# Optimization experiments

Measured on AMD Instinct MI355X. Metric: run time of the kernel, lower is better.

The kernel has to match this reference:

```python
import jax, jax.numpy as jnp
import numpy as np

D_MODEL = 1024
NHEAD = 16
HEAD_DIM = D_MODEL // NHEAD


def setup_inputs() -> dict:
    key = jax.random.key(0)
    ks = jax.random.split(key, 11)
    B, L, D = 4, 2048, D_MODEL
    s = 1.0 / np.sqrt(D)  # ~ torch Linear init scale
    return {
        "queries": jax.random.normal(ks[0], (B, L, D), jnp.float32),
        "keys": jax.random.normal(ks[1], (B, L, D), jnp.float32),
        "values": jax.random.normal(ks[2], (B, L, D), jnp.float32),
        "Wq": jax.random.normal(ks[3], (D, D), jnp.float32) * s,
        "bq": jnp.zeros((D,), jnp.float32),
        "Wk": jax.random.normal(ks[4], (D, D), jnp.float32) * s,
        "bk": jnp.zeros((D,), jnp.float32),
        "Wv": jax.random.normal(ks[5], (D, D), jnp.float32) * s,
        "bv": jnp.zeros((D,), jnp.float32),
        "Wo": jax.random.normal(ks[6], (D, D), jnp.float32) * s,
        "bo": jnp.zeros((D,), jnp.float32),
    }


def reference(queries, keys, values, Wq, bq, Wk, bk, Wv, bv, Wo, bo):
    B, L, D = queries.shape
    H, dh = NHEAD, HEAD_DIM
    # projections (W stored as [in, out])
    q = (queries @ Wq + bq).reshape(B, L, H, dh).transpose(0, 2, 1, 3)  # [B,H,L,dh]
    k = (keys @ Wk + bk).reshape(B, L, H, dh).transpose(0, 2, 1, 3)
    v = (values @ Wv + bv).reshape(B, L, H, dh).transpose(0, 2, 1, 3)
    scores = jnp.einsum("bhqd,bhkd->bhqk", q, k) / jnp.sqrt(jnp.float32(dh))
    attn = jax.nn.softmax(scores, axis=-1)  # dropout p=0 -> identity
    ctx = jnp.einsum("bhqk,bhkd->bhqd", attn, v)
    ctx = ctx.transpose(0, 2, 1, 3).reshape(B, L, D)
    return ctx @ Wo + bo
```

## Files before the change

### kernel.cpp

```cpp
#include <hip/hip_runtime.h>
#include <math.h>


using f32x4 = __attribute__((ext_vector_type(4))) float;
using bf16x8 = __attribute__((ext_vector_type(8))) short;

__device__ __forceinline__ unsigned short f2bf(float x) {
  union { float f; unsigned u; } v; v.f = x;
  unsigned r = v.u + 0x7fff + ((v.u >> 16) & 1);
  return (unsigned short)(r >> 16);
}

__device__ __forceinline__ void g2l16(const void* g, void* l) {
  __builtin_amdgcn_global_load_lds(
      (const __attribute__((address_space(1))) unsigned int*)g,
      (__attribute__((address_space(3))) unsigned int*)l, 16, 0, 0);
}

__global__ __launch_bounds__(256) void wt4_k(const float* __restrict__ W0,
                                             const float* __restrict__ W1,
                                             const float* __restrict__ W2,
                                             const float* __restrict__ W3,
                                             short* __restrict__ WT) {
  __shared__ float t[64][65];
  const int z = blockIdx.z;
  const float* W = z == 0 ? W0 : (z == 1 ? W1 : (z == 2 ? W2 : W3));
  short* hiT = WT + (size_t)z * 1048576;
  const int n0 = blockIdx.x * 64, k0 = blockIdx.y * 64;
  const int tid = threadIdx.x;
  const int r = tid >> 4, c4 = (tid & 15) * 4;
#pragma unroll
  for (int i = 0; i < 4; i++) {
    const int row = r + i * 16;
    const float4 v = *(const float4*)&W[(size_t)(k0 + row) * 1024 + n0 + c4];
    t[c4 + 0][row] = v.x;
    t[c4 + 1][row] = v.y;
    t[c4 + 2][row] = v.z;
    t[c4 + 3][row] = v.w;
  }
  __syncthreads();
#pragma unroll
  for (int i = 0; i < 4; i++) {
    const int row = r + i * 16;
    short4 h;
    h.x = (short)f2bf(t[row][c4 + 0]);
    h.y = (short)f2bf(t[row][c4 + 1]);
    h.z = (short)f2bf(t[row][c4 + 2]);
    h.w = (short)f2bf(t[row][c4 + 3]);
    *(short4*)&hiT[(size_t)(n0 + row) * 1024 + k0 + c4] = h;
  }
}

__global__ __launch_bounds__(256) void cvt3_k(const float* __restrict__ A0,
                                              const float* __restrict__ A1,
                                              const float* __restrict__ A2,
                                              short* __restrict__ X) {
  const int z = blockIdx.y;
  const float* A = z == 0 ? A0 : (z == 1 ? A1 : A2);
  short* Xo = X + (size_t)z * 8388608;
  const int t0 = blockIdx.x * 256 + threadIdx.x;
#pragma unroll 2
  for (int i = t0; i < 1048576; i += 262144) {
    const size_t o = (size_t)i * 8;
    const float4 a = *(const float4*)&A[o];
    const float4 b = *(const float4*)&A[o + 4];
    short tmp[8];
    tmp[0] = (short)f2bf(a.x);
    tmp[1] = (short)f2bf(a.y);
    tmp[2] = (short)f2bf(a.z);
    tmp[3] = (short)f2bf(a.w);
    tmp[4] = (short)f2bf(b.x);
    tmp[5] = (short)f2bf(b.y);
    tmp[6] = (short)f2bf(b.z);
    tmp[7] = (short)f2bf(b.w);
    *(bf16x8*)&Xo[o] = *(const bf16x8*)tmp;
  }
}

__global__ __launch_bounds__(256, 4) void proj3_k(
    const short* __restrict__ X, const short* __restrict__ WT,
    const float* __restrict__ b0, const float* __restrict__ b1,
    const float* __restrict__ b2, short* __restrict__ Obase) {
  __shared__ short smem[64 * 144];
  short* As = smem;
  short* Bs = smem + 4096;

  const int z = blockIdx.z;
  const short* A_g = X + (size_t)z * 8388608;
  const short* B_g = WT + (size_t)z * 1048576;
  const float* bias = z == 0 ? b0 : (z == 1 ? b1 : b2);
  short* outp = Obase + (size_t)z * 8388608;

  const int tid = threadIdx.x;
  const int lane = tid & 63;
  const int wave = tid >> 6;
  const int quad = lane >> 4;
  const int l16 = lane & 15;
  const int m0 = blockIdx.x * 128;
  const int n0 = blockIdx.y * 128;
  const int wm = (wave >> 1) * 64;
  const int wn = (wave & 1) * 64;

  const int srow = tid >> 2;
  const int soff = (tid & 3) * 8;

  f32x4 acc[4][4];
#pragma unroll
  for (int i = 0; i < 4; i++)
#pragma unroll
    for (int j = 0; j < 4; j++) acc[i][j] = f32x4{0.f, 0.f, 0.f, 0.f};

  for (int k0 = 0; k0 < 1024; k0 += 32) {
    __syncthreads();
#pragma unroll
    for (int i = 0; i < 2; i++) {
      const int row = srow + i * 64;
      g2l16(&A_g[(size_t)(m0 + row) * 1024 + k0 + soff], &As[row * 32 + soff]);
      g2l16(&B_g[(size_t)(n0 + row) * 1024 + k0 + soff], &Bs[row * 32 + soff]);
    }
    __syncthreads();

    bf16x8 ah[4], bh[4];
#pragma unroll
    for (int t = 0; t < 4; t++) {
      ah[t] = *(const bf16x8*)&As[(wm + t * 16 + l16) * 32 + quad * 8];
      bh[t] = *(const bf16x8*)&Bs[(wn + t * 16 + l16) * 32 + quad * 8];
    }
#pragma unroll
    for (int tm = 0; tm < 4; tm++)
#pragma unroll
      for (int tn = 0; tn < 4; tn++)
        acc[tm][tn] = __builtin_amdgcn_mfma_f32_16x16x32_bf16(ah[tm], bh[tn], acc[tm][tn], 0, 0, 0);
  }

  float bz[4];
#pragma unroll
  for (int tn = 0; tn < 4; tn++) bz[tn] = bias[n0 + wn + tn * 16 + l16];
  const float sc = (z == 0) ? 0.125f : 1.0f;

  const int b = m0 >> 11;
  const int lbase = m0 & 2047;

  if (z == 2) {
#pragma unroll
    for (int half = 0; half < 2; half++) {
      __syncthreads();
      if ((wave & 1) == half) {
#pragma unroll
        for (int tm = 0; tm < 4; tm++)
#pragma unroll
          for (int tn = 0; tn < 4; tn++)
#pragma unroll
            for (int r = 0; r < 4; r++) {
              const int nl = tn * 16 + l16;
              const int ml = wm + tm * 16 + quad * 4 + r;
              smem[nl * 144 + ml] = (short)f2bf(acc[tm][tn][r] + bz[tn]);
            }
      }
      __syncthreads();
      const int h = (n0 >> 6) + half;
#pragma unroll
      for (int j = 0; j < 4; j++) {
        const int c = tid + j * 256;
        const int d = c >> 4;
        const int mo = (c & 15) * 8;
        *(bf16x8*)&outp[((size_t)((b * 16 + h) * 64 + d)) * 2048 + lbase + mo] =
            *(const bf16x8*)&smem[d * 144 + mo];
      }
    }
  } else {
#pragma unroll
    for (int half = 0; half < 2; half++) {
      __syncthreads();
      if ((wave & 1) == half) {
#pragma unroll
        for (int tm = 0; tm < 4; tm++)
#pragma unroll
          for (int tn = 0; tn < 4; tn++)
#pragma unroll
            for (int r = 0; r < 4; r++) {
              const int ml = wm + tm * 16 + quad * 4 + r;
              const int nl = tn * 16 + l16;
              smem[ml * 72 + nl] = (short)f2bf((acc[tm][tn][r] + bz[tn]) * sc);
            }
      }
      __syncthreads();
      const int h = (n0 >> 6) + half;
#pragma unroll
      for (int j = 0; j < 4; j++) {
        const int c = tid + j * 256;
        const int ml = c >> 3;
        const int off = (c & 7) * 8;
        *(bf16x8*)&outp[((size_t)(b * 16 + h) * 2048 + lbase + ml) * 64 + off] =
            *(const bf16x8*)&smem[ml * 72 + off];
      }
    }
  }
}

__global__ __launch_bounds__(256, 2) void outproj_k(
    const short* __restrict__ A_g, const short* __restrict__ B_g,
    const float* __restrict__ bias, float* __restrict__ out0) {
  __shared__ short As[4096];
  __shared__ short Bs[4096];

  const int tid = threadIdx.x;
  const int lane = tid & 63;
  const int wave = tid >> 6;
  const int quad = lane >> 4;
  const int l16 = lane & 15;
  const int m0 = blockIdx.x * 128;
  const int n0 = blockIdx.y * 128;
  const int wm = (wave >> 1) * 64;
  const int wn = (wave & 1) * 64;
  const int srow = tid >> 2;
  const int soff = (tid & 3) * 8;

  f32x4 acc[4][4];
#pragma unroll
  for (int i = 0; i < 4; i++)
#pragma unroll
    for (int j = 0; j < 4; j++) acc[i][j] = f32x4{0.f, 0.f, 0.f, 0.f};

  for (int k0 = 0; k0 < 1024; k0 += 32) {
    __syncthreads();
#pragma unroll
    for (int i = 0; i < 2; i++) {
      const int row = srow + i * 64;
      g2l16(&A_g[(size_t)(m0 + row) * 1024 + k0 + soff], &As[row * 32 + soff]);
      g2l16(&B_g[(size_t)(n0 + row) * 1024 + k0 + soff], &Bs[row * 32 + soff]);
    }
    __syncthreads();

    bf16x8 ah[4], bh[4];
#pragma unroll
    for (int t = 0; t < 4; t++) {
      ah[t] = *(const bf16x8*)&As[(wm + t * 16 + l16) * 32 + quad * 8];
      bh[t] = *(const bf16x8*)&Bs[(wn + t * 16 + l16) * 32 + quad * 8];
    }
#pragma unroll
    for (int tm = 0; tm < 4; tm++)
#pragma unroll
      for (int tn = 0; tn < 4; tn++)
        acc[tm][tn] = __builtin_amdgcn_mfma_f32_16x16x32_bf16(ah[tm], bh[tn], acc[tm][tn], 0, 0, 0);
  }

  float bz[4];
#pragma unroll
  for (int tn = 0; tn < 4; tn++) bz[tn] = bias[n0 + wn + tn * 16 + l16];

#pragma unroll
  for (int tm = 0; tm < 4; tm++)
#pragma unroll
    for (int tn = 0; tn < 4; tn++) {
      const int n = n0 + wn + tn * 16 + l16;
#pragma unroll
      for (int r = 0; r < 4; r++) {
        const int m = m0 + wm + tm * 16 + quad * 4 + r;
        out0[(size_t)m * 1024 + n] = acc[tm][tn][r] + bz[tn];
      }
    }
}

__global__ __launch_bounds__(256, 4) void attn3_k(const short* __restrict__ Qp,
                                                  const short* __restrict__ Kp,
                                                  const short* __restrict__ Vt,
                                                  short* __restrict__ Ctx) {
  __shared__ short Ks[64 * 72];
  __shared__ short Vs[64 * 72];
  __shared__ short Ps[128 * 72];

  const int tid = threadIdx.x;
  const int lane = tid & 63;
  const int wave = tid >> 6;
  const int quad = lane >> 4;
  const int l16 = lane & 15;
  const int bh = blockIdx.x;
  const int q0 = blockIdx.y * 128;

  const short* Kb = Kp + (size_t)bh * 2048 * 64;
  const short* Vb = Vt + (size_t)bh * 64 * 2048;

  bf16x8 qf[2][2];
#pragma unroll
  for (int s = 0; s < 2; s++) {
    const short* qp =
        Qp + ((size_t)bh * 2048 + q0 + wave * 32 + s * 16 + l16) * 64 + quad * 8;
    qf[s][0] = *(const bf16x8*)qp;
    qf[s][1] = *(const bf16x8*)(qp + 32);
  }

  bf16x8 ones;
#pragma unroll
  for (int j = 0; j < 8; j++) ones[j] = (short)0x3F80;

  f32x4 O[2][4], lacc[2];
#pragma unroll
  for (int s = 0; s < 2; s++) {
    lacc[s] = f32x4{0.f, 0.f, 0.f, 0.f};
#pragma unroll
    for (int jo = 0; jo < 4; jo++) O[s][jo] = f32x4{0.f, 0.f, 0.f, 0.f};
  }

  const int srow0 = tid >> 3, soff = (tid & 7) * 8;
  const int srow1 = (tid + 256) >> 3;

  bf16x8 kreg[2], vreg[2];
  kreg[0] = *(const bf16x8*)&Kb[(size_t)srow0 * 64 + soff];
  kreg[1] = *(const bf16x8*)&Kb[(size_t)srow1 * 64 + soff];
  vreg[0] = *(const bf16x8*)&Vb[(size_t)srow0 * 2048 + soff];
  vreg[1] = *(const bf16x8*)&Vb[(size_t)srow1 * 2048 + soff];

  for (int kt = 0; kt < 32; kt++) {
    __syncthreads();
    *(bf16x8*)&Ks[srow0 * 72 + soff] = kreg[0];
    *(bf16x8*)&Ks[srow1 * 72 + soff] = kreg[1];
    *(bf16x8*)&Vs[srow0 * 72 + soff] = vreg[0];
    *(bf16x8*)&Vs[srow1 * 72 + soff] = vreg[1];
    __syncthreads();

    if (kt < 31) {
      const int nb = (kt + 1) * 64;
      kreg[0] = *(const bf16x8*)&Kb[(size_t)(nb + srow0) * 64 + soff];
      kreg[1] = *(const bf16x8*)&Kb[(size_t)(nb + srow1) * 64 + soff];
      vreg[0] = *(const bf16x8*)&Vb[(size_t)srow0 * 2048 + nb + soff];
      vreg[1] = *(const bf16x8*)&Vb[(size_t)srow1 * 2048 + nb + soff];
    }

#pragma unroll
    for (int s = 0; s < 2; s++) {
      f32x4 sacc[4];
#pragma unroll
      for (int j = 0; j < 4; j++) sacc[j] = f32x4{0.f, 0.f, 0.f, 0.f};
#pragma unroll
      for (int c = 0; c < 2; c++)
#pragma unroll
        for (int j = 0; j < 4; j++) {
          const bf16x8 kf = *(const bf16x8*)&Ks[(j * 16 + l16) * 72 + c * 32 + quad * 8];
          sacc[j] = __builtin_amdgcn_mfma_f32_16x16x32_bf16(qf[s][c], kf, sacc[j], 0, 0, 0);
        }
#pragma unroll
      for (int j = 0; j < 4; j++)
#pragma unroll
        for (int r = 0; r < 4; r++) {
          const float e = __expf(sacc[j][r]);
          Ps[(wave * 32 + s * 16 + quad * 4 + r) * 72 + j * 16 + l16] =
              (short)(__float_as_uint(e) >> 16);
        }
    }

#pragma unroll
    for (int c = 0; c < 2; c++) {
      const bf16x8 pf0 = *(const bf16x8*)&Ps[(wave * 32 + l16) * 72 + c * 32 + quad * 8];
      const bf16x8 pf1 = *(const bf16x8*)&Ps[(wave * 32 + 16 + l16) * 72 + c * 32 + quad * 8];
      lacc[0] = __builtin_amdgcn_mfma_f32_16x16x32_bf16(pf0, ones, lacc[0], 0, 0, 0);
      lacc[1] = __builtin_amdgcn_mfma_f32_16x16x32_bf16(pf1, ones, lacc[1], 0, 0, 0);
#pragma unroll
      for (int jo = 0; jo < 4; jo++) {
        const bf16x8 vf = *(const bf16x8*)&Vs[(jo * 16 + l16) * 72 + c * 32 + quad * 8];
        O[0][jo] = __builtin_amdgcn_mfma_f32_16x16x32_bf16(pf0, vf, O[0][jo], 0, 0, 0);
        O[1][jo] = __builtin_amdgcn_mfma_f32_16x16x32_bf16(pf1, vf, O[1][jo], 0, 0, 0);
      }
    }
  }

  const int b = bh >> 4, h = bh & 15;
#pragma unroll
  for (int s = 0; s < 2; s++)
#pragma unroll
    for (int r = 0; r < 4; r++) {
      const float inv_l = 1.0f / lacc[s][r];
      const size_t row = (size_t)b * 2048 + q0 + wave * 32 + s * 16 + quad * 4 + r;
#pragma unroll
      for (int jo = 0; jo < 4; jo++)
        Ctx[row * 1024 + h * 64 + jo * 16 + l16] = (short)f2bf(O[s][jo][r] * inv_l);
    }
}

extern "C" void kernel_launch(void* const* d_in, const int* in_sizes, int n_in,
                              void* d_out, int out_size, void* d_ws, size_t ws_size,
                              hipStream_t stream) {
  const float* queries = (const float*)d_in[0];
  const float* keys    = (const float*)d_in[1];
  const float* values  = (const float*)d_in[2];
  const float* Wq = (const float*)d_in[3];
  const float* bq = (const float*)d_in[4];
  const float* Wk = (const float*)d_in[5];
  const float* bk = (const float*)d_in[6];
  const float* Wv = (const float*)d_in[7];
  const float* bv = (const float*)d_in[8];
  const float* Wo = (const float*)d_in[9];
  const float* bo = (const float*)d_in[10];
  float* out = (float*)d_out;

  const size_t PLANE = (size_t)8192 * 1024 * 2;
  const size_t WPL = (size_t)1024 * 1024 * 2;

  char* p = (char*)d_ws;
  short* WT  = (short*)p;  p += 4 * WPL;
  short* X   = (short*)p;  p += 3 * PLANE;
  short* Qp  = (short*)p;  p += PLANE;
  short* Kp  = (short*)p;  p += PLANE;
  short* Vt  = (short*)p;  p += PLANE;
  short* ctx = X;
  (void)Kp;

  const dim3 blk(256);
  wt4_k<<<dim3(16, 16, 4), blk, 0, stream>>>(Wq, Wk, Wv, Wo, WT);
  cvt3_k<<<dim3(1024, 3), blk, 0, stream>>>(queries, keys, values, X);

  proj3_k<<<dim3(64, 8, 3), blk, 0, stream>>>(X, WT, bq, bk, bv, Qp);

  attn3_k<<<dim3(64, 16), blk, 0, stream>>>(Qp, Kp, Vt, ctx);

  outproj_k<<<dim3(64, 8), blk, 0, stream>>>(ctx, WT + 3 * 1048576, bo, out);
}
```

Before: 384.1 us.

## Rewrite attention with 32x32 MFMA, register-resident P, and swizzled LDS

```diff
diff --git a/kernel.cpp b/kernel.cpp
--- a/kernel.cpp
+++ b/kernel.cpp
@@ -3,6 +3,7 @@
 
 
 using f32x4 = __attribute__((ext_vector_type(4))) float;
+using f32x16 = __attribute__((ext_vector_type(16))) float;
 using bf16x8 = __attribute__((ext_vector_type(8))) short;
 
 __device__ __forceinline__ unsigned short f2bf(float x) {
@@ -136,7 +137,7 @@
   float bz[4];
 #pragma unroll
   for (int tn = 0; tn < 4; tn++) bz[tn] = bias[n0 + wn + tn * 16 + l16];
-  const float sc = (z == 0) ? 0.125f : 1.0f;
+  const float sc = (z == 0) ? 0.18033688011112f : 1.0f;
 
   const int b = m0 >> 11;
   const int lbase = m0 & 2047;
@@ -262,119 +263,125 @@
     }
 }
 
-__global__ __launch_bounds__(256, 4) void attn3_k(const short* __restrict__ Qp,
+__global__ __launch_bounds__(256, 4) void attn4_k(const short* __restrict__ Qp,
                                                   const short* __restrict__ Kp,
                                                   const short* __restrict__ Vt,
                                                   short* __restrict__ Ctx) {
-  __shared__ short Ks[64 * 72];
-  __shared__ short Vs[64 * 72];
-  __shared__ short Ps[128 * 72];
+  __shared__ short Ks[64 * 64];
+  __shared__ short Vs[64 * 64];
 
   const int tid = threadIdx.x;
   const int lane = tid & 63;
   const int wave = tid >> 6;
-  const int quad = lane >> 4;
-  const int l16 = lane & 15;
+  const int l31 = lane & 31;
+  const int hh = lane >> 5;
   const int bh = blockIdx.x;
   const int q0 = blockIdx.y * 128;
 
   const short* Kb = Kp + (size_t)bh * 2048 * 64;
   const short* Vb = Vt + (size_t)bh * 64 * 2048;
 
-  bf16x8 qf[2][2];
-#pragma unroll
-  for (int s = 0; s < 2; s++) {
-    const short* qp =
-        Qp + ((size_t)bh * 2048 + q0 + wave * 32 + s * 16 + l16) * 64 + quad * 8;
-    qf[s][0] = *(const bf16x8*)qp;
-    qf[s][1] = *(const bf16x8*)(qp + 32);
-  }
-
-  bf16x8 ones;
-#pragma unroll
-  for (int j = 0; j < 8; j++) ones[j] = (short)0x3F80;
-
-  f32x4 O[2][4], lacc[2];
-#pragma unroll
-  for (int s = 0; s < 2; s++) {
-    lacc[s] = f32x4{0.f, 0.f, 0.f, 0.f};
-#pragma unroll
-    for (int jo = 0; jo < 4; jo++) O[s][jo] = f32x4{0.f, 0.f, 0.f, 0.f};
-  }
-
-  const int srow0 = tid >> 3, soff = (tid & 7) * 8;
-  const int srow1 = (tid + 256) >> 3;
+  bf16x8 qf[4];
+#pragma unroll
+  for (int dseg = 0; dseg < 4; dseg++)
+    qf[dseg] = *(const bf16x8*)
+        &Qp[((size_t)bh * 2048 + q0 + wave * 32 + l31) * 64 + dseg * 16 + hh * 8];
+
+  f32x16 O[2];
+#pragma unroll
+  for (int t = 0; t < 2; t++)
+#pragma unroll
+    for (int r = 0; r < 16; r++) O[t][r] = 0.0f;
+  float lrow = 0.0f;
+
+  const int srow0 = tid >> 3;
+  const int srow1 = srow0 + 32;
+  const int scol = (tid & 7) * 8;
+  const int w0 = srow0 * 64 + (scol ^ ((srow0 & 7) << 3));
+  const int w1 = srow1 * 64 + (scol ^ ((srow1 & 7) << 3));
 
   bf16x8 kreg[2], vreg[2];
-  kreg[0] = *(const bf16x8*)&Kb[(size_t)srow0 * 64 + soff];
-  kreg[1] = *(const bf16x8*)&Kb[(size_t)srow1 * 64 + soff];
-  vreg[0] = *(const bf16x8*)&Vb[(size_t)srow0 * 2048 + soff];
-  vreg[1] = *(const bf16x8*)&Vb[(size_t)srow1 * 2048 + soff];
+  kreg[0] = *(const bf16x8*)&Kb[(size_t)srow0 * 64 + scol];
+  kreg[1] = *(const bf16x8*)&Kb[(size_t)srow1 * 64 + scol];
+  vreg[0] = *(const bf16x8*)&Vb[(size_t)srow0 * 2048 + scol];
+  vreg[1] = *(const bf16x8*)&Vb[(size_t)srow1 * 2048 + scol];
 
   for (int kt = 0; kt < 32; kt++) {
     __syncthreads();
-    *(bf16x8*)&Ks[srow0 * 72 + soff] = kreg[0];
-    *(bf16x8*)&Ks[srow1 * 72 + soff] = kreg[1];
-    *(bf16x8*)&Vs[srow0 * 72 + soff] = vreg[0];
-    *(bf16x8*)&Vs[srow1 * 72 + soff] = vreg[1];
+    *(bf16x8*)&Ks[w0] = kreg[0];
+    *(bf16x8*)&Ks[w1] = kreg[1];
+    *(bf16x8*)&Vs[w0] = vreg[0];
+    *(bf16x8*)&Vs[w1] = vreg[1];
     __syncthreads();
 
     if (kt < 31) {
       const int nb = (kt + 1) * 64;
-      kreg[0] = *(const bf16x8*)&Kb[(size_t)(nb + srow0) * 64 + soff];
-      kreg[1] = *(const bf16x8*)&Kb[(size_t)(nb + srow1) * 64 + soff];
-      vreg[0] = *(const bf16x8*)&Vb[(size_t)srow0 * 2048 + nb + soff];
-      vreg[1] = *(const bf16x8*)&Vb[(size_t)srow1 * 2048 + nb + soff];
-    }
-
-#pragma unroll
-    for (int s = 0; s < 2; s++) {
-      f32x4 sacc[4];
-#pragma unroll
-      for (int j = 0; j < 4; j++) sacc[j] = f32x4{0.f, 0.f, 0.f, 0.f};
-#pragma unroll
-      for (int c = 0; c < 2; c++)
-#pragma unroll
-        for (int j = 0; j < 4; j++) {
-          const bf16x8 kf = *(const bf16x8*)&Ks[(j * 16 + l16) * 72 + c * 32 + quad * 8];
-          sacc[j] = __builtin_amdgcn_mfma_f32_16x16x32_bf16(qf[s][c], kf, sacc[j], 0, 0, 0);
+      kreg[0] = *(const bf16x8*)&Kb[(size_t)(nb + srow0) * 64 + scol];
+      kreg[1] = *(const bf16x8*)&Kb[(size_t)(nb + srow1) * 64 + scol];
+      vreg[0] = *(const bf16x8*)&Vb[(size_t)srow0 * 2048 + nb + scol];
+      vreg[1] = *(const bf16x8*)&Vb[(size_t)srow1 * 2048 + nb + scol];
+    }
+
+#pragma unroll
+    for (int kc = 0; kc < 2; kc++) {
+      f32x16 s;
+#pragma unroll
+      for (int r = 0; r < 16; r++) s[r] = 0.0f;
+#pragma unroll
+      for (int dseg = 0; dseg < 4; dseg++) {
+        const int kr = kc * 32 + l31;
+        const bf16x8 kf = *(const bf16x8*)
+            &Ks[kr * 64 + ((dseg * 16 + hh * 8) ^ ((kr & 7) << 3))];
+        s = __builtin_amdgcn_mfma_f32_32x32x16_bf16(kf, qf[dseg], s, 0, 0, 0);
+      }
+#pragma unroll
+      for (int r = 0; r < 16; r++) {
+        s[r] = exp2f(s[r]);
+        lrow += s[r];
+      }
+      unsigned p[8];
+#pragma unroll
+      for (int i = 0; i < 8; i++) {
+        const float lo = s[2 * i], hi = s[2 * i + 1];
+        unsigned d;
+        asm("v_cvt_pk_bf16_f32 %0, %1, %2" : "=v"(d) : "v"(lo), "v"(hi));
+        p[i] = d;
+      }
+      asm("v_permlane32_swap_b32 %0, %1" : "+v"(p[0]), "+v"(p[2]));
+      asm("v_permlane32_swap_b32 %0, %1" : "+v"(p[1]), "+v"(p[3]));
+      asm("v_permlane32_swap_b32 %0, %1" : "+v"(p[4]), "+v"(p[6]));
+      asm("v_permlane32_swap_b32 %0, %1" : "+v"(p[5]), "+v"(p[7]));
+#pragma unroll
+      for (int kk = 0; kk < 2; kk++) {
+        union { unsigned u[4]; bf16x8 v; } pa;
+        pa.u[0] = p[kk * 4 + 0];
+        pa.u[1] = p[kk * 4 + 1];
+        pa.u[2] = p[kk * 4 + 2];
+        pa.u[3] = p[kk * 4 + 3];
+#pragma unroll
+        for (int t = 0; t < 2; t++) {
+          const int vr = t * 32 + l31;
+          const bf16x8 vf = *(const bf16x8*)
+              &Vs[vr * 64 + ((((kc * 2 + kk) * 16) + hh * 8) ^ ((vr & 7) << 3))];
+          O[t] = __builtin_amdgcn_mfma_f32_32x32x16_bf16(pa.v, vf, O[t], 0, 0, 0);
         }
-#pragma unroll
-      for (int j = 0; j < 4; j++)
-#pragma unroll
-        for (int r = 0; r < 4; r++) {
-          const float e = __expf(sacc[j][r]);
-          Ps[(wave * 32 + s * 16 + quad * 4 + r) * 72 + j * 16 + l16] =
-              (short)(__float_as_uint(e) >> 16);
-        }
-    }
-
-#pragma unroll
-    for (int c = 0; c < 2; c++) {
-      const bf16x8 pf0 = *(const bf16x8*)&Ps[(wave * 32 + l16) * 72 + c * 32 + quad * 8];
-      const bf16x8 pf1 = *(const bf16x8*)&Ps[(wave * 32 + 16 + l16) * 72 + c * 32 + quad * 8];
-      lacc[0] = __builtin_amdgcn_mfma_f32_16x16x32_bf16(pf0, ones, lacc[0], 0, 0, 0);
-      lacc[1] = __builtin_amdgcn_mfma_f32_16x16x32_bf16(pf1, ones, lacc[1], 0, 0, 0);
-#pragma unroll
-      for (int jo = 0; jo < 4; jo++) {
-        const bf16x8 vf = *(const bf16x8*)&Vs[(jo * 16 + l16) * 72 + c * 32 + quad * 8];
-        O[0][jo] = __builtin_amdgcn_mfma_f32_16x16x32_bf16(pf0, vf, O[0][jo], 0, 0, 0);
-        O[1][jo] = __builtin_amdgcn_mfma_f32_16x16x32_bf16(pf1, vf, O[1][jo], 0, 0, 0);
-      }
-    }
-  }
-
-  const int b = bh >> 4, h = bh & 15;
-#pragma unroll
-  for (int s = 0; s < 2; s++)
-#pragma unroll
-    for (int r = 0; r < 4; r++) {
-      const float inv_l = 1.0f / lacc[s][r];
-      const size_t row = (size_t)b * 2048 + q0 + wave * 32 + s * 16 + quad * 4 + r;
-#pragma unroll
-      for (int jo = 0; jo < 4; jo++)
-        Ctx[row * 1024 + h * 64 + jo * 16 + l16] = (short)f2bf(O[s][jo][r] * inv_l);
-    }
+      }
+    }
+  }
+
+  const float linv = 1.0f / (lrow + __shfl_xor(lrow, 32));
+
+  const int bq = bh >> 4, head = bh & 15;
+  const size_t rowbase = (size_t)bq * 2048 + q0 + wave * 32;
+#pragma unroll
+  for (int r = 0; r < 16; r++) {
+    const int qrow = (r & 3) + 8 * (r >> 2) + 4 * hh;
+    const float inv = __shfl(linv, qrow);
+#pragma unroll
+    for (int t = 0; t < 2; t++)
+      Ctx[(rowbase + qrow) * 1024 + head * 64 + t * 32 + l31] =
+          (short)f2bf(O[t][r] * inv);
+  }
 }
 
 extern "C" void kernel_launch(void* const* d_in, const int* in_sizes, int n_in,
@@ -411,7 +418,7 @@
 
   proj3_k<<<dim3(64, 8, 3), blk, 0, stream>>>(X, WT, bq, bk, bv, Qp);
 
-  attn3_k<<<dim3(64, 16), blk, 0, stream>>>(Qp, Kp, Vt, ctx);
+  attn4_k<<<dim3(64, 16), blk, 0, stream>>>(Qp, Kp, Vt, ctx);
 
   outproj_k<<<dim3(64, 8), blk, 0, stream>>>(ctx, WT + 3 * 1048576, bo, out);
 }
```

New measurement: 374.0 us. 2.6% less time.
